# Kernel tuning notes

Measured on AMD Instinct MI355X. Metric: run time of the kernel, lower is better.

## Reference

```python
import jax, jax.numpy as jnp
import numpy as np

# Geometry (LLaMA-7B-like attention)
B, H, S, D = 1, 32, 2048, 128
NUM_ELEM = B * H * S * D
NUM_OUTLIERS = NUM_ELEM // 256   # outlier_ratio = 1/256 -> 32768 outliers
SINK_LENGTH = 4                  # first 4 tokens of V kept in full precision
QMAX = 7.0                       # symmetric int4: values in [-8, 7]
EPS = 1e-6


def setup_inputs() -> dict:
    key = jax.random.key(0)
    kq, kk, kv = jax.random.split(key, 3)
    q = jax.random.normal(kq, (B, H, S, D), dtype=jnp.float32)
    k = jax.random.normal(kk, (B, H, S, D), dtype=jnp.float32)
    v = jax.random.normal(kv, (B, H, S, D), dtype=jnp.float32)
    return {"q": q, "k": k, "v": v}


def _isolate(x):
    """Split x into dense (outliers zeroed) + sparse (top-|x| values, flat indices)."""
    flat = x.reshape(-1)
    _, idx = jax.lax.top_k(jnp.abs(flat), NUM_OUTLIERS)
    sp_val = flat[idx]
    dense = flat.at[idx].set(0.0).reshape(x.shape)
    return dense, sp_val, idx


def _sink_flat_indices():
    # flat indices of v[:, :, :SINK_LENGTH, :] in row-major [B,H,S,D] layout
    b = jnp.arange(B)[:, None, None, None]
    h = jnp.arange(H)[None, :, None, None]
    s = jnp.arange(SINK_LENGTH)[None, None, :, None]
    d = jnp.arange(D)[None, None, None, :]
    return (((b * H + h) * S + s) * D + d).reshape(-1)


def _quant_dequant(x, scale):
    # symmetric round-to-nearest int4 quantize, then dequantize
    q = jnp.clip(jnp.round(x / scale), -8.0, QMAX)
    return q * scale


def reference(q, k, v):
    # 1) Outlier isolation (K along tokens, V along channels; both flattened scatter)
    k_dense, k_sp_val, k_sp_idx = _isolate(k)
    v_dense, v_sp_val, v_sp_idx = _isolate(v)

    # 2) Sink-token isolation for V (chunk_idx == 0 path): zero sinks in dense,
    #    append their fp values/indices to the sparse set
    sink_idx = _sink_flat_indices()
    v_flat = v.reshape(-1)
    sink_values = v_flat[sink_idx]
    v_dense = v_dense.reshape(-1).at[sink_idx].set(0.0).reshape(v.shape)
    v_sp_val = jnp.concatenate([v_sp_val, sink_values])
    v_sp_idx = jnp.concatenate([v_sp_idx, sink_idx])

    # 3) Per-(head, channel) scale stats (EMA init == first-chunk max |.|)
    k_scale = jnp.maximum(jnp.max(jnp.abs(k_dense), axis=(0, 2), keepdims=True), EPS) / QMAX
    v_scale = jnp.maximum(jnp.max(jnp.abs(v_dense), axis=(0, 2), keepdims=True), EPS) / QMAX

    # 4) Quantize dense part, then reconstruct cache entries: dequant + sparse restore
    k_rec = _quant_dequant(k_dense, k_scale)
    v_rec = _quant_dequant(v_dense, v_scale)
    k_rec = k_rec.reshape(-1).at[k_sp_idx].set(k_sp_val).reshape(k.shape)
    v_rec = v_rec.reshape(-1).at[v_sp_idx].set(v_sp_val).reshape(v.shape)

    # 5) Causal attention over reconstructed KV cache
    scale = 1.0 / np.sqrt(D).astype(np.float32)
    scores = jnp.einsum('bhqd,bhkd->bhqk', q, k_rec) * scale
    causal = jnp.tril(jnp.ones((S, S), dtype=bool))
    scores = jnp.where(causal[None, None], scores, jnp.finfo(scores.dtype).min)
    attn = jax.nn.softmax(scores, axis=-1)
    out = jnp.einsum('bhqk,bhkd->bhqd', attn, v_rec)
    return out
```

## Files before the change

kernel.cpp:

```cpp
#include <hip/hip_runtime.h>

typedef unsigned short u16;
typedef unsigned int u32;
typedef unsigned long long u64;
typedef __attribute__((ext_vector_type(8))) short short8;
typedef __attribute__((ext_vector_type(4))) float f32x4;

#define N_ELEM 8388608
#define NH 32
#define SEQ 2048
#define HD 128
#define KTOP 32768u
#define CAND_CAP 8192u

__device__ __forceinline__ u16 f2bf(float f) {
  union { float f; u32 u; } v; v.f = f;
  u32 r = v.u + 0x7fffu + ((v.u >> 16) & 1u);
  return (u16)(r >> 16);
}

__device__ __forceinline__ float dqf(float x, u32 t, u64 Kr, u32 idx, bool sink, float scale) {
  union { float f; u32 u; } w; w.f = x;
  const u32 ab = w.u & 0x7fffffffu;
  const u32 bin = ab >> 16;
  const bool keep = sink || (bin > t) ||
                    (bin == t && ((((u64)ab) << 32) | (u32)(~idx)) >= Kr);
  if (keep) return x;
  float q = rintf(x / scale);
  q = fminf(fmaxf(q, -8.0f), 7.0f);
  return q * scale;
}

template<int CTRL>
__device__ __forceinline__ float dppmov(float x) {
  union { float f; int i; } a, b;
  a.f = x;
  b.i = __builtin_amdgcn_mov_dpp(a.i, CTRL, 0xF, 0xF, true);
  return b.f;
}
__device__ __forceinline__ float rowmax16(float x) {
  x = fmaxf(x, dppmov<0xB1>(x));
  x = fmaxf(x, dppmov<0x4E>(x));
  x = fmaxf(x, dppmov<0x141>(x));
  x = fmaxf(x, dppmov<0x140>(x));
  return x;
}
__device__ __forceinline__ float rowsum16(float x) {
  x += dppmov<0xB1>(x);
  x += dppmov<0x4E>(x);
  x += dppmov<0x141>(x);
  x += dppmov<0x140>(x);
  return x;
}

__global__ __launch_bounds__(256) void hist_kernel(const float* __restrict__ k,
                                                   const float* __restrict__ v,
                                                   u32* __restrict__ histK,
                                                   u32* __restrict__ histV) {
  __shared__ u32 sh[16384];
  const int tensor = blockIdx.x >> 7;
  const int bid = blockIdx.x & 127;
  const float* src = tensor ? v : k;
  u32* gh = tensor ? histV : histK;
  for (int i = threadIdx.x; i < 16384; i += 256) sh[i] = 0;
  __syncthreads();
  const int per = N_ELEM / 128;
  const int base = bid * per;
  for (int i = threadIdx.x; i < per / 4; i += 256) {
    f32x4 x = *(const f32x4*)(src + base + i * 4);
#pragma unroll
    for (int j = 0; j < 4; ++j) {
      union { float f; u32 u; } w; w.f = x[j];
      u32 b = (w.u & 0x7fffffffu) >> 16;
      atomicAdd(&sh[b >> 1], 1u << ((b & 1u) * 16));
    }
  }
  __syncthreads();
  for (int i = threadIdx.x; i < 16384; i += 256) {
    u32 w = sh[i];
    u32 lo = w & 0xffffu, hi = w >> 16;
    if (lo) atomicAdd(&gh[2 * i], lo);
    if (hi) atomicAdd(&gh[2 * i + 1], hi);
  }
}

__global__ __launch_bounds__(256) void thresh_kernel(const u32* __restrict__ histK,
                                                     const u32* __restrict__ histV,
                                                     u32* __restrict__ ctrl) {
  const u32* hist = blockIdx.x ? histV : histK;
  u32* c = ctrl + blockIdx.x * 8;
  __shared__ u32 part[256];
  __shared__ u32 bins[128];
  __shared__ u32 sh_chunk, sh_cum;
  u32 s = 0;
  for (int i = 0; i < 128; ++i) s += hist[threadIdx.x * 128 + i];
  part[threadIdx.x] = s;
  __syncthreads();
  if (threadIdx.x == 0) {
    u32 cum = 0;
    int chunk = 255;
    while (chunk > 0 && cum + part[chunk] < KTOP) { cum += part[chunk]; --chunk; }
    sh_chunk = (u32)chunk; sh_cum = cum;
  }
  __syncthreads();
  const u32 chunk = sh_chunk;
  if (threadIdx.x < 128) bins[threadIdx.x] = hist[chunk * 128 + threadIdx.x];
  __syncthreads();
  if (threadIdx.x == 0) {
    u32 cum = sh_cum;
    int b = 127;
    while (b > 0 && cum + bins[b] < KTOP) { cum += bins[b]; --b; }
    c[0] = chunk * 128 + (u32)b;
    c[1] = KTOP - cum;
  }
}

__global__ __launch_bounds__(256) void candmax_kernel(const float* __restrict__ k,
                                                      const float* __restrict__ v,
                                                      u32* __restrict__ ctrl,
                                                      u32* __restrict__ caK, u32* __restrict__ ciK,
                                                      u32* __restrict__ caV, u32* __restrict__ ciV,
                                                      u32* __restrict__ kmax,
                                                      u32* __restrict__ vmax) {
  __shared__ u32 colmax[128];
  const int tensor = blockIdx.y;
  const float* src = tensor ? v : k;
  u32* ca = tensor ? caV : caK;
  u32* ci = tensor ? ciV : ciK;
  u32* cnt = &ctrl[tensor * 8 + 4];
  u32* mbuf = tensor ? vmax : kmax;
  const u32 t = ctrl[tensor * 8 + 0];
  const int h = blockIdx.x >> 3;
  const int q8 = blockIdx.x & 7;
  const int tid = threadIdx.x;
  if (tid < 128) colmax[tid] = 0;
  __syncthreads();
  const int c0 = 4 * (tid & 31);
  u32 mx[4] = {0, 0, 0, 0};
  for (int p = 0; p < 32; ++p) {
    const int s = q8 * 256 + p * 8 + (tid >> 5);
    const u32 idx = ((u32)(h * SEQ + s) << 7) + (u32)c0;
    f32x4 x = *(const f32x4*)(src + idx);
    const bool skipmax = (tensor == 1 && s < 4);
#pragma unroll
    for (int j = 0; j < 4; ++j) {
      union { float f; u32 u; } w; w.f = x[j];
      const u32 ab = w.u & 0x7fffffffu;
      const u32 bin = ab >> 16;
      if (bin == t) {
        u32 slot = atomicAdd(cnt, 1u);
        if (slot < CAND_CAP) { ca[slot] = ab; ci[slot] = idx + j; }
      }
      if (bin < t && !skipmax && ab > mx[j]) mx[j] = ab;
    }
  }
#pragma unroll
  for (int j = 0; j < 4; ++j) atomicMax(&colmax[c0 + j], mx[j]);
  __syncthreads();
  if (tid < 128) atomicMax(&mbuf[h * HD + tid], colmax[tid]);
}

__global__ __launch_bounds__(256) void ksel_kernel(u32* __restrict__ ctrl,
                                                   const u32* __restrict__ caK, const u32* __restrict__ ciK,
                                                   const u32* __restrict__ caV, const u32* __restrict__ ciV) {
  __shared__ u64 keys[CAND_CAP];
  const int tensor = blockIdx.y;
  u32* c = ctrl + tensor * 8;
  const u32 r = c[1];
  u32 T = c[4];
  if (T > CAND_CAP) T = CAND_CAP;
  const u32* ca = tensor ? caV : caK;
  const u32* ci = tensor ? ciV : ciK;
  for (u32 j = threadIdx.x; j < T; j += 256)
    keys[j] = (((u64)ca[j]) << 32) | (u32)(~ci[j]);
  __syncthreads();
  for (u32 i = blockIdx.x * 256 + threadIdx.x; i < T; i += 32 * 256) {
    const u64 ki = keys[i];
    u32 cnt = 0;
    for (u32 j = 0; j < T; ++j) cnt += (keys[j] > ki) ? 1u : 0u;
    if (cnt == r - 1) { c[2] = (u32)(ki >> 32); c[3] = (u32)ki; }
  }
}

__global__ __launch_bounds__(256) void maxfix_scale_kernel(const u32* __restrict__ ctrl,
                                                           const u32* __restrict__ caK, const u32* __restrict__ ciK,
                                                           const u32* __restrict__ caV, const u32* __restrict__ ciV,
                                                           u32* __restrict__ kmax, u32* __restrict__ vmax,
                                                           float* __restrict__ kscale, float* __restrict__ vscale) {
  const int tensor = blockIdx.x;
  const u32* c = ctrl + tensor * 8;
  const u64 Kr = (((u64)c[2]) << 32) | c[3];
  u32 T = c[4];
  if (T > CAND_CAP) T = CAND_CAP;
  const u32* ca = tensor ? caV : caK;
  const u32* ci = tensor ? ciV : ciK;
  u32* mbuf = tensor ? vmax : kmax;
  for (u32 i = threadIdx.x; i < T; i += 256) {
    const u32 ab = ca[i], idx = ci[i];
    const u64 key = (((u64)ab) << 32) | (u32)(~idx);
    if (key >= Kr) continue;
    if (tensor == 1 && ((idx >> 7) & 2047) < 4) continue;
    atomicMax(&mbuf[(idx >> 18) * HD + (idx & 127)], ab);
  }
  __syncthreads();
  float* sbuf = tensor ? vscale : kscale;
  for (int i = threadIdx.x; i < NH * HD; i += 256) {
    union { u32 u; float f; } a; a.u = mbuf[i];
    sbuf[i] = fmaxf(a.f, 1e-6f) / 7.0f;
  }
}

__global__ __launch_bounds__(256) void recon_k_kernel(const float* __restrict__ K,
                                                      const u32* __restrict__ ctrl,
                                                      const float* __restrict__ kscale,
                                                      u16* __restrict__ krec) {
  const u32 t = ctrl[0];
  const u64 Kr = (((u64)ctrl[2]) << 32) | ctrl[3];
  const int stride = gridDim.x * 256;
  for (int i = blockIdx.x * 256 + threadIdx.x; i < N_ELEM / 4; i += stride) {
    const u32 e = (u32)i * 4;
    const u32 d0 = e & 127, h = e >> 18;
    f32x4 x = *(const f32x4*)(K + e);
    f32x4 sc = *(const f32x4*)(kscale + h * HD + d0);
    u16 y[4];
#pragma unroll
    for (int j = 0; j < 4; ++j) y[j] = f2bf(dqf(x[j], t, Kr, e + j, false, sc[j]));
    *(u32*)(krec + e) = ((u32)y[0]) | (((u32)y[1]) << 16);
    *(u32*)(krec + e + 2) = ((u32)y[2]) | (((u32)y[3]) << 16);
  }
}

__global__ __launch_bounds__(256) void recon_vt_kernel(const float* __restrict__ V,
                                                       const u32* __restrict__ ctrl,
                                                       const float* __restrict__ vscale,
                                                       u16* __restrict__ vrecT) {
  __shared__ u32 ld[64][65];
  const u32 t = ctrl[8];
  const u64 Kr = (((u64)ctrl[10]) << 32) | ctrl[11];
  const int h = blockIdx.x, sb = blockIdx.y;
  const int tid = threadIdx.x;
  const int d0 = 4 * (tid & 31);
  f32x4 sc = *(const f32x4*)(vscale + h * HD + d0);
#pragma unroll
  for (int p = 0; p < 8; ++p) {
    const int sl = p * 8 + (tid >> 5);
    const int tok = sb * 64 + sl;
    const bool sink = tok < 4;
    const u32 idx = ((u32)(h * SEQ + tok) << 7) + (u32)d0;
    f32x4 x = *(const f32x4*)(V + idx);
    u16 y[4];
#pragma unroll
    for (int j = 0; j < 4; ++j) y[j] = f2bf(dqf(x[j], t, Kr, idx + j, sink, sc[j]));
    ld[(d0 >> 1)][sl] = ((u32)y[0]) | (((u32)y[1]) << 16);
    ld[(d0 >> 1) + 1][sl] = ((u32)y[2]) | (((u32)y[3]) << 16);
  }
  __syncthreads();
  const int d = tid >> 1, so = (tid & 1) * 32, e = d & 1;
  u16* outp = vrecT + (size_t)(h * 32 + sb) * 8192 + d * 64 + so;
#pragma unroll
  for (int i = 0; i < 4; ++i) {
    short8 y;
#pragma unroll
    for (int m = 0; m < 8; ++m) {
      const u32 w2 = ld[d >> 1][so + i * 8 + m];
      y[m] = (short)(u16)(w2 >> (16 * e));
    }
    *(short8*)(outp + i * 8) = y;
  }
}

__global__ __launch_bounds__(256, 2) void flash_pre(const float* __restrict__ Q,
                                                    const u16* __restrict__ krec,
                                                    const u16* __restrict__ vrecT,
                                                    float* __restrict__ Out) {
  __shared__ u16 ks[64][136];
  __shared__ u16 vt[128][72];
  __shared__ u16 pl[4][16][72];

  const int blk = blockIdx.x;
  const int h = blk >> 4;
  const int pa = blk & 15;
  const int RA = pa << 6;
  const int RB = (31 - pa) << 6;
  const int tid = threadIdx.x;
  const int w = tid >> 6, lane = tid & 63;
  const int l16 = lane & 15, quad = lane >> 4;
  const float SC = 0.12751743f;
  const float NEG = -30000.0f;

  short8 qf[2][4];
#pragma unroll
  for (int m = 0; m < 2; ++m) {
    const int R = m ? RB : RA;
    const float* qp = Q + ((size_t)(h * SEQ + R + w * 16 + l16)) * HD + quad * 8;
#pragma unroll
    for (int c = 0; c < 4; ++c) {
      f32x4 a = *(const f32x4*)(qp + c * 32);
      f32x4 b = *(const f32x4*)(qp + c * 32 + 4);
#pragma unroll
      for (int j = 0; j < 4; ++j) {
        qf[m][c][j] = (short)f2bf(a[j]);
        qf[m][c][4 + j] = (short)f2bf(b[j]);
      }
    }
  }

  f32x4 o[2][8];
  float mrow[2][4], lrow[2][4];
#pragma unroll
  for (int m = 0; m < 2; ++m) {
#pragma unroll
    for (int i = 0; i < 8; ++i) o[m][i] = (f32x4){0.f, 0.f, 0.f, 0.f};
#pragma unroll
    for (int r = 0; r < 4; ++r) { mrow[m][r] = NEG; lrow[m][r] = 0.f; }
  }

  const int krow = tid >> 2, kqo = (tid & 3) * 32;
  const int vd = tid >> 1, vso = (tid & 1) * 32;
  const u16* kbase = krec + ((size_t)h * SEQ + krow) * HD + kqo;
  const u16* vbase = vrecT + (size_t)h * 32 * 8192 + vd * 64 + vso;
  short8 kr[4], vr[4];
#pragma unroll
  for (int i = 0; i < 4; ++i) kr[i] = *(const short8*)(kbase + i * 8);
#pragma unroll
  for (int i = 0; i < 4; ++i) vr[i] = *(const short8*)(vbase + i * 8);

  const int ktiles = (RB >> 6) + 1;
  for (int kt = 0; kt < ktiles; ++kt) {
    const int kb = kt << 6;
    __syncthreads();
#pragma unroll
    for (int i = 0; i < 4; ++i) *(short8*)(&ks[krow][kqo + i * 8]) = kr[i];
#pragma unroll
    for (int i = 0; i < 4; ++i) *(short8*)(&vt[vd][vso + i * 8]) = vr[i];
    __syncthreads();
    if (kt + 1 < ktiles) {
      const u16* kp = kbase + (size_t)(kt + 1) * 64 * HD;
      const u16* vp = vbase + (size_t)(kt + 1) * 8192;
#pragma unroll
      for (int i = 0; i < 4; ++i) kr[i] = *(const short8*)(kp + i * 8);
#pragma unroll
      for (int i = 0; i < 4; ++i) vr[i] = *(const short8*)(vp + i * 8);
    }
#pragma unroll
    for (int m = 0; m < 2; ++m) {
      const int R = m ? RB : RA;
      if (kb > R) continue;
      f32x4 sa[4];
#pragma unroll
      for (int ni = 0; ni < 4; ++ni) {
        f32x4 acc = (f32x4){0.f, 0.f, 0.f, 0.f};
#pragma unroll
        for (int c = 0; c < 4; ++c) {
          short8 kf = *(const short8*)(&ks[ni * 16 + l16][c * 32 + quad * 8]);
          acc = __builtin_amdgcn_mfma_f32_16x16x32_bf16(qf[m][c], kf, acc, 0, 0, 0);
        }
        sa[ni] = acc;
      }
      const bool diag = (kb == R);
#pragma unroll
      for (int ni = 0; ni < 4; ++ni)
#pragma unroll
        for (int r = 0; r < 4; ++r) {
          float sv = sa[ni][r] * SC;
          if (diag && (ni * 16 + l16) > (w * 16 + quad * 4 + r)) sv = NEG;
          sa[ni][r] = sv;
        }
      float alpha[4];
#pragma unroll
      for (int r = 0; r < 4; ++r) {
        float mx = fmaxf(fmaxf(sa[0][r], sa[1][r]), fmaxf(sa[2][r], sa[3][r]));
        mx = rowmax16(mx);
        const float mn = fmaxf(mrow[m][r], mx);
        alpha[r] = exp2f(mrow[m][r] - mn);
        mrow[m][r] = mn;
        float sum = 0.f;
#pragma unroll
        for (int ni = 0; ni < 4; ++ni) {
          const float p = exp2f(sa[ni][r] - mn);
          sa[ni][r] = p;
          sum += p;
        }
        sum = rowsum16(sum);
        lrow[m][r] = lrow[m][r] * alpha[r] + sum;
      }
#pragma unroll
      for (int ni = 0; ni < 4; ++ni)
#pragma unroll
        for (int r = 0; r < 4; ++r)
          pl[w][quad * 4 + r][ni * 16 + l16] = f2bf(sa[ni][r]);
#pragma unroll
      for (int i = 0; i < 8; ++i)
#pragma unroll
        for (int r = 0; r < 4; ++r) o[m][i][r] *= alpha[r];
#pragma unroll
      for (int kc = 0; kc < 2; ++kc) {
        short8 af = *(const short8*)(&pl[w][l16][kc * 32 + quad * 8]);
#pragma unroll
        for (int ds = 0; ds < 8; ++ds) {
          short8 vf = *(const short8*)(&vt[ds * 16 + l16][kc * 32 + quad * 8]);
          o[m][ds] = __builtin_amdgcn_mfma_f32_16x16x32_bf16(af, vf, o[m][ds], 0, 0, 0);
        }
      }
    }
  }
#pragma unroll
  for (int m = 0; m < 2; ++m) {
    const int R = m ? RB : RA;
#pragma unroll
    for (int r = 0; r < 4; ++r) {
      const float inv = 1.0f / lrow[m][r];
      const int qr = R + w * 16 + quad * 4 + r;
      float* op = Out + ((size_t)(h * SEQ + qr)) * HD + l16;
#pragma unroll
      for (int ds = 0; ds < 8; ++ds) op[ds * 16] = o[m][ds][r] * inv;
    }
  }
}

__global__ __launch_bounds__(256, 2) void flash_fb(const float* __restrict__ Q,
                                                   const float* __restrict__ K,
                                                   const float* __restrict__ V,
                                                   const u32* __restrict__ ctrl,
                                                   const float* __restrict__ kscale,
                                                   const float* __restrict__ vscale,
                                                   float* __restrict__ Out) {
  __shared__ u16 ks[64][136];
  __shared__ u16 vt[128][72];
  __shared__ u16 pl[4][16][72];
  const int blk = blockIdx.x;
  const int h = blk >> 5;
  const int qt = 31 - (blk & 31);
  const int qb = qt << 6;
  const int tid = threadIdx.x;
  const int w = tid >> 6, lane = tid & 63;
  const int l16 = lane & 15, quad = lane >> 4;
  const float SM_SCALE = 0.08838834764831843f;
  const float NEG = -30000.0f;
  const u32 tK = ctrl[0];
  const u64 KrK = (((u64)ctrl[2]) << 32) | ctrl[3];
  const u32 tV = ctrl[8];
  const u64 KrV = (((u64)ctrl[10]) << 32) | ctrl[11];
  const int cch = (tid & 15) * 8;
  float ksc[8], vsc[8];
#pragma unroll
  for (int j = 0; j < 8; ++j) {
    ksc[j] = kscale[h * HD + cch + j];
    vsc[j] = vscale[h * HD + cch + j];
  }
  short8 qf[4];
  {
    const float* qp = Q + ((size_t)(h * SEQ + qb + w * 16 + l16)) * HD + quad * 8;
#pragma unroll
    for (int c = 0; c < 4; ++c) {
      f32x4 a = *(const f32x4*)(qp + c * 32);
      f32x4 b = *(const f32x4*)(qp + c * 32 + 4);
#pragma unroll
      for (int j = 0; j < 4; ++j) {
        qf[c][j] = (short)f2bf(a[j]);
        qf[c][4 + j] = (short)f2bf(b[j]);
      }
    }
  }
  f32x4 o[8];
#pragma unroll
  for (int i = 0; i < 8; ++i) o[i] = (f32x4){0.f, 0.f, 0.f, 0.f};
  float mrow[4], lrow[4];
#pragma unroll
  for (int r = 0; r < 4; ++r) { mrow[r] = NEG; lrow[r] = 0.f; }
  const int ktiles = qt + 1;
  for (int kt = 0; kt < ktiles; ++kt) {
    const int kb = kt << 6;
    __syncthreads();
    {
      const int r0 = tid >> 4;
      const float* kp = K + (size_t)(h * SEQ + kb) * HD;
#pragma unroll
      for (int i = 0; i < 4; ++i) {
        const int row = r0 + i * 16;
        f32x4 x0 = *(const f32x4*)(kp + (size_t)row * HD + cch);
        f32x4 x1 = *(const f32x4*)(kp + (size_t)row * HD + cch + 4);
        const u32 bidx = ((u32)(h * SEQ + kb + row) << 7) + (u32)cch;
        short8 yv;
#pragma unroll
        for (int j = 0; j < 4; ++j) {
          yv[j]     = (short)f2bf(dqf(x0[j], tK, KrK, bidx + j,     false, ksc[j]));
          yv[4 + j] = (short)f2bf(dqf(x1[j], tK, KrK, bidx + 4 + j, false, ksc[4 + j]));
        }
        *(short8*)(&ks[row][cch]) = yv;
      }
    }
    {
      const float* vp = V + (size_t)(h * SEQ + kb) * HD;
#pragma unroll
      for (int i = 0; i < 4; ++i) {
        const int tchunk = tid + i * 256;
        const int s = tchunk >> 4;
        const int tok = kb + s;
        const bool sink = tok < 4;
        f32x4 x0 = *(const f32x4*)(vp + (size_t)s * HD + cch);
        f32x4 x1 = *(const f32x4*)(vp + (size_t)s * HD + cch + 4);
        const u32 bidx = ((u32)(h * SEQ + tok) << 7) + (u32)cch;
#pragma unroll
        for (int j = 0; j < 4; ++j) {
          vt[cch + j][s]     = f2bf(dqf(x0[j], tV, KrV, bidx + j,     sink, vsc[j]));
          vt[cch + 4 + j][s] = f2bf(dqf(x1[j], tV, KrV, bidx + 4 + j, sink, vsc[4 + j]));
        }
      }
    }
    __syncthreads();
    f32x4 sa[4];
#pragma unroll
    for (int ni = 0; ni < 4; ++ni) {
      f32x4 acc = (f32x4){0.f, 0.f, 0.f, 0.f};
#pragma unroll
      for (int c = 0; c < 4; ++c) {
        short8 kf = *(const short8*)(&ks[ni * 16 + l16][c * 32 + quad * 8]);
        acc = __builtin_amdgcn_mfma_f32_16x16x32_bf16(qf[c], kf, acc, 0, 0, 0);
      }
      sa[ni] = acc;
    }
    const bool diag = (kb == qb);
#pragma unroll
    for (int ni = 0; ni < 4; ++ni)
#pragma unroll
      for (int r = 0; r < 4; ++r) {
        float sv = sa[ni][r] * SM_SCALE;
        if (diag) {
          const int qr = w * 16 + quad * 4 + r;
          const int kc = ni * 16 + l16;
          if (kc > qr) sv = NEG;
        }
        sa[ni][r] = sv;
      }
    float alpha[4];
#pragma unroll
    for (int r = 0; r < 4; ++r) {
      float mx = fmaxf(fmaxf(sa[0][r], sa[1][r]), fmaxf(sa[2][r], sa[3][r]));
      mx = fmaxf(mx, __shfl_xor(mx, 1));
      mx = fmaxf(mx, __shfl_xor(mx, 2));
      mx = fmaxf(mx, __shfl_xor(mx, 4));
      mx = fmaxf(mx, __shfl_xor(mx, 8));
      const float mn = fmaxf(mrow[r], mx);
      alpha[r] = __expf(mrow[r] - mn);
      mrow[r] = mn;
      float sum = 0.f;
#pragma unroll
      for (int ni = 0; ni < 4; ++ni) {
        const float p = __expf(sa[ni][r] - mn);
        sa[ni][r] = p;
        sum += p;
      }
      sum += __shfl_xor(sum, 1);
      sum += __shfl_xor(sum, 2);
      sum += __shfl_xor(sum, 4);
      sum += __shfl_xor(sum, 8);
      lrow[r] = lrow[r] * alpha[r] + sum;
    }
#pragma unroll
    for (int ni = 0; ni < 4; ++ni)
#pragma unroll
      for (int r = 0; r < 4; ++r)
        pl[w][quad * 4 + r][ni * 16 + l16] = f2bf(sa[ni][r]);
    __syncthreads();
#pragma unroll
    for (int i = 0; i < 8; ++i)
#pragma unroll
      for (int r = 0; r < 4; ++r) o[i][r] *= alpha[r];
#pragma unroll
    for (int kc = 0; kc < 2; ++kc) {
      short8 af = *(const short8*)(&pl[w][l16][kc * 32 + quad * 8]);
#pragma unroll
      for (int ds = 0; ds < 8; ++ds) {
        short8 vf = *(const short8*)(&vt[ds * 16 + l16][kc * 32 + quad * 8]);
        o[ds] = __builtin_amdgcn_mfma_f32_16x16x32_bf16(af, vf, o[ds], 0, 0, 0);
      }
    }
  }
#pragma unroll
  for (int r = 0; r < 4; ++r) {
    const float inv = 1.0f / lrow[r];
    const int qr = qb + w * 16 + quad * 4 + r;
    float* op = Out + ((size_t)(h * SEQ + qr)) * HD + l16;
#pragma unroll
    for (int ds = 0; ds < 8; ++ds) op[ds * 16] = o[ds][r] * inv;
  }
}

extern "C" void kernel_launch(void* const* d_in, const int* in_sizes, int n_in,
                              void* d_out, int out_size, void* d_ws, size_t ws_size,
                              hipStream_t stream) {
  const float* q = (const float*)d_in[0];
  const float* k = (const float*)d_in[1];
  const float* v = (const float*)d_in[2];
  float* out = (float*)d_out;
  char* ws = (char*)d_ws;

  u32* ctrl    = (u32*)ws;
  u32* histK   = (u32*)(ws + 256);
  u32* histV   = (u32*)(ws + 256 + 131072);
  u32* kmax    = (u32*)(ws + 262400);
  u32* vmax    = (u32*)(ws + 278784);
  const size_t ZERO_BYTES = 295168;
  float* kscale = (float*)(ws + 295168);
  float* vscale = (float*)(ws + 311552);
  u32* caK = (u32*)(ws + 327936);
  u32* ciK = caK + CAND_CAP;
  u32* caV = ciK + CAND_CAP;
  u32* ciV = caV + CAND_CAP;
  u16* krec  = (u16*)(ws + 458752);
  u16* vrecT = (u16*)(ws + 458752 + 16777216);
  const size_t NEED = 458752 + 2ull * 16777216;

  hipMemsetAsync(ws, 0, ZERO_BYTES, stream);
  hist_kernel<<<256, 256, 0, stream>>>(k, v, histK, histV);
  thresh_kernel<<<2, 256, 0, stream>>>(histK, histV, ctrl);
  candmax_kernel<<<dim3(256, 2), 256, 0, stream>>>(k, v, ctrl, caK, ciK, caV, ciV, kmax, vmax);
  ksel_kernel<<<dim3(32, 2), 256, 0, stream>>>(ctrl, caK, ciK, caV, ciV);
  maxfix_scale_kernel<<<2, 256, 0, stream>>>(ctrl, caK, ciK, caV, ciV, kmax, vmax, kscale, vscale);
  if (ws_size >= NEED) {
    recon_k_kernel<<<2048, 256, 0, stream>>>(k, ctrl, kscale, krec);
    recon_vt_kernel<<<dim3(32, 32), 256, 0, stream>>>(v, ctrl, vscale, vrecT);
    flash_pre<<<512, 256, 0, stream>>>(q, krec, vrecT, out);
  } else {
    flash_fb<<<32 * 32, 256, 0, stream>>>(q, k, v, ctrl, kscale, vscale, out);
  }
}
```

Before: 362.3 us.

## Compute transposed S tile so P stays in registers, dropping the LDS round-trip

Flash_pre now computes S^T with K as the A operand, so each lane owns one query row. Row max and sum need only two cross-lane shuffles, and P is packed to bf16 with v_cvt_pk_bf16_f32 and fed straight into the PV MFMA, removing the pl shared-memory staging. K rows are permuted when written to LDS so the register layout of P lines up with the V operand. The two query tiles are interleaved to raise MFMA ILP, and alpha and l are redistributed with ds_bpermute, at the cost of more register pressure and a subtle layout permutation that must stay correct.

```diff
diff --git a/kernel.cpp b/kernel.cpp
--- a/kernel.cpp
+++ b/kernel.cpp
@@ -31,26 +31,17 @@
   return q * scale;
 }
 
-template<int CTRL>
-__device__ __forceinline__ float dppmov(float x) {
+__device__ __forceinline__ u32 cvtpk_bf16(float lo, float hi) {
+  u32 r;
+  asm("v_cvt_pk_bf16_f32 %0, %1, %2" : "=v"(r) : "v"(lo), "v"(hi));
+  return r;
+}
+
+__device__ __forceinline__ float bperm_f(int ibyte, float x) {
   union { float f; int i; } a, b;
   a.f = x;
-  b.i = __builtin_amdgcn_mov_dpp(a.i, CTRL, 0xF, 0xF, true);
+  b.i = __builtin_amdgcn_ds_bpermute(ibyte, a.i);
   return b.f;
-}
-__device__ __forceinline__ float rowmax16(float x) {
-  x = fmaxf(x, dppmov<0xB1>(x));
-  x = fmaxf(x, dppmov<0x4E>(x));
-  x = fmaxf(x, dppmov<0x141>(x));
-  x = fmaxf(x, dppmov<0x140>(x));
-  return x;
-}
-__device__ __forceinline__ float rowsum16(float x) {
-  x += dppmov<0xB1>(x);
-  x += dppmov<0x4E>(x);
-  x += dppmov<0x141>(x);
-  x += dppmov<0x140>(x);
-  return x;
 }
 
 __global__ __launch_bounds__(256) void hist_kernel(const float* __restrict__ k,
@@ -269,13 +260,58 @@
   }
 }
 
+#define SC_QK 0.12751743f
+#define NEGS -30000.0f
+
+__device__ __forceinline__ void softmax_pack(f32x4 s[4], float& mrow, float& lrow,
+                                             u32 pk[8], f32x4& av, bool diag,
+                                             int qrow16, int quad, const int* idxR) {
+#pragma unroll
+  for (int ni = 0; ni < 4; ++ni)
+#pragma unroll
+    for (int r = 0; r < 4; ++r) {
+      float sv = s[ni][r] * SC_QK;
+      const int tokl = ((ni >> 1) << 5) | (quad << 3) | ((ni & 1) << 2) | r;
+      if (diag && tokl > qrow16) sv = NEGS;
+      s[ni][r] = sv;
+    }
+  float m01 = fmaxf(fmaxf(fmaxf(s[0][0], s[0][1]), fmaxf(s[0][2], s[0][3])),
+                    fmaxf(fmaxf(s[1][0], s[1][1]), fmaxf(s[1][2], s[1][3])));
+  float m23 = fmaxf(fmaxf(fmaxf(s[2][0], s[2][1]), fmaxf(s[2][2], s[2][3])),
+                    fmaxf(fmaxf(s[3][0], s[3][1]), fmaxf(s[3][2], s[3][3])));
+  float mx = fmaxf(m01, m23);
+  mx = fmaxf(mx, __shfl_xor(mx, 16));
+  mx = fmaxf(mx, __shfl_xor(mx, 32));
+  const float mn = fmaxf(mrow, mx);
+  const float al = exp2f(mrow - mn);
+  mrow = mn;
+  float sum = 0.f;
+#pragma unroll
+  for (int ni = 0; ni < 4; ++ni)
+#pragma unroll
+    for (int r = 0; r < 4; ++r) {
+      const float p = exp2f(s[ni][r] - mn);
+      s[ni][r] = p;
+      sum += p;
+    }
+  sum += __shfl_xor(sum, 16);
+  sum += __shfl_xor(sum, 32);
+  lrow = lrow * al + sum;
+#pragma unroll
+  for (int ni = 0; ni < 4; ++ni) {
+    pk[ni * 2] = cvtpk_bf16(s[ni][0], s[ni][1]);
+    pk[ni * 2 + 1] = cvtpk_bf16(s[ni][2], s[ni][3]);
+  }
+#pragma unroll
+  for (int r = 0; r < 4; ++r) av[r] = bperm_f(idxR[r], al);
+}
+
 __global__ __launch_bounds__(256, 2) void flash_pre(const float* __restrict__ Q,
                                                     const u16* __restrict__ krec,
                                                     const u16* __restrict__ vrecT,
                                                     float* __restrict__ Out) {
   __shared__ u16 ks[64][136];
   __shared__ u16 vt[128][72];
-  __shared__ u16 pl[4][16][72];
 
   const int blk = blockIdx.x;
   const int h = blk >> 4;
@@ -285,8 +321,11 @@
   const int tid = threadIdx.x;
   const int w = tid >> 6, lane = tid & 63;
   const int l16 = lane & 15, quad = lane >> 4;
-  const float SC = 0.12751743f;
-  const float NEG = -30000.0f;
+  const int qrow16 = w * 16 + l16;
+
+  int idxR[4];
+#pragma unroll
+  for (int r = 0; r < 4; ++r) idxR[r] = ((lane & 48) | (quad * 4 + r)) << 2;
 
   short8 qf[2][4];
 #pragma unroll
@@ -297,25 +336,27 @@
     for (int c = 0; c < 4; ++c) {
       f32x4 a = *(const f32x4*)(qp + c * 32);
       f32x4 b = *(const f32x4*)(qp + c * 32 + 4);
-#pragma unroll
-      for (int j = 0; j < 4; ++j) {
-        qf[m][c][j] = (short)f2bf(a[j]);
-        qf[m][c][4 + j] = (short)f2bf(b[j]);
-      }
+      union { u32 u[4]; short8 v; } t;
+      t.u[0] = cvtpk_bf16(a[0], a[1]);
+      t.u[1] = cvtpk_bf16(a[2], a[3]);
+      t.u[2] = cvtpk_bf16(b[0], b[1]);
+      t.u[3] = cvtpk_bf16(b[2], b[3]);
+      qf[m][c] = t.v;
     }
   }
 
   f32x4 o[2][8];
-  float mrow[2][4], lrow[2][4];
+  float mrow[2], lrow[2];
 #pragma unroll
   for (int m = 0; m < 2; ++m) {
 #pragma unroll
     for (int i = 0; i < 8; ++i) o[m][i] = (f32x4){0.f, 0.f, 0.f, 0.f};
-#pragma unroll
-    for (int r = 0; r < 4; ++r) { mrow[m][r] = NEG; lrow[m][r] = 0.f; }
+    mrow[m] = NEGS; lrow[m] = 0.f;
   }
 
   const int krow = tid >> 2, kqo = (tid & 3) * 32;
+  const int krp = (krow & 35) | (((krow >> 2) & 1) << 4) |
+                  (((krow >> 4) & 1) << 3) | (((krow >> 3) & 1) << 2);
   const int vd = tid >> 1, vso = (tid & 1) * 32;
   const u16* kbase = krec + ((size_t)h * SEQ + krow) * HD + kqo;
   const u16* vbase = vrecT + (size_t)h * 32 * 8192 + vd * 64 + vso;
@@ -330,7 +371,7 @@
     const int kb = kt << 6;
     __syncthreads();
 #pragma unroll
-    for (int i = 0; i < 4; ++i) *(short8*)(&ks[krow][kqo + i * 8]) = kr[i];
+    for (int i = 0; i < 4; ++i) *(short8*)(&ks[krp][kqo + i * 8]) = kr[i];
 #pragma unroll
     for (int i = 0; i < 4; ++i) *(short8*)(&vt[vd][vso + i * 8]) = vr[i];
     __syncthreads();
@@ -342,78 +383,89 @@
 #pragma unroll
       for (int i = 0; i < 4; ++i) vr[i] = *(const short8*)(vp + i * 8);
     }
-#pragma unroll
-    for (int m = 0; m < 2; ++m) {
-      const int R = m ? RB : RA;
-      if (kb > R) continue;
-      f32x4 sa[4];
+    const bool actA = (kb <= RA);
+
+    f32x4 s0[4], s1[4];
+    if (actA) {
 #pragma unroll
       for (int ni = 0; ni < 4; ++ni) {
-        f32x4 acc = (f32x4){0.f, 0.f, 0.f, 0.f};
+        f32x4 a0 = (f32x4){0.f, 0.f, 0.f, 0.f};
+        f32x4 a1 = (f32x4){0.f, 0.f, 0.f, 0.f};
 #pragma unroll
         for (int c = 0; c < 4; ++c) {
           short8 kf = *(const short8*)(&ks[ni * 16 + l16][c * 32 + quad * 8]);
-          acc = __builtin_amdgcn_mfma_f32_16x16x32_bf16(qf[m][c], kf, acc, 0, 0, 0);
+          a0 = __builtin_amdgcn_mfma_f32_16x16x32_bf16(kf, qf[0][c], a0, 0, 0, 0);
+          a1 = __builtin_amdgcn_mfma_f32_16x16x32_bf16(kf, qf[1][c], a1, 0, 0, 0);
         }
-        sa[ni] = acc;
-      }
-      const bool diag = (kb == R);
-#pragma unroll
-      for (int ni = 0; ni < 4; ++ni)
-#pragma unroll
-        for (int r = 0; r < 4; ++r) {
-          float sv = sa[ni][r] * SC;
-          if (diag && (ni * 16 + l16) > (w * 16 + quad * 4 + r)) sv = NEG;
-          sa[ni][r] = sv;
+        s0[ni] = a0; s1[ni] = a1;
+      }
+    } else {
+#pragma unroll
+      for (int ni = 0; ni < 4; ++ni) {
+        f32x4 a1 = (f32x4){0.f, 0.f, 0.f, 0.f};
+#pragma unroll
+        for (int c = 0; c < 4; ++c) {
+          short8 kf = *(const short8*)(&ks[ni * 16 + l16][c * 32 + quad * 8]);
+          a1 = __builtin_amdgcn_mfma_f32_16x16x32_bf16(kf, qf[1][c], a1, 0, 0, 0);
         }
-      float alpha[4];
-#pragma unroll
-      for (int r = 0; r < 4; ++r) {
-        float mx = fmaxf(fmaxf(sa[0][r], sa[1][r]), fmaxf(sa[2][r], sa[3][r]));
-        mx = rowmax16(mx);
-        const float mn = fmaxf(mrow[m][r], mx);
-        alpha[r] = exp2f(mrow[m][r] - mn);
-        mrow[m][r] = mn;
-        float sum = 0.f;
-#pragma unroll
-        for (int ni = 0; ni < 4; ++ni) {
-          const float p = exp2f(sa[ni][r] - mn);
-          sa[ni][r] = p;
-          sum += p;
-        }
-        sum = rowsum16(sum);
-        lrow[m][r] = lrow[m][r] * alpha[r] + sum;
-      }
-#pragma unroll
-      for (int ni = 0; ni < 4; ++ni)
-#pragma unroll
-        for (int r = 0; r < 4; ++r)
-          pl[w][quad * 4 + r][ni * 16 + l16] = f2bf(sa[ni][r]);
-#pragma unroll
-      for (int i = 0; i < 8; ++i)
-#pragma unroll
-        for (int r = 0; r < 4; ++r) o[m][i][r] *= alpha[r];
+        s1[ni] = a1;
+      }
+    }
+
+    u32 pk0[8], pk1[8];
+    f32x4 av0, av1;
+    if (actA) softmax_pack(s0, mrow[0], lrow[0], pk0, av0, kb == RA, qrow16, quad, idxR);
+    softmax_pack(s1, mrow[1], lrow[1], pk1, av1, kb == RB, qrow16, quad, idxR);
+
+    if (actA) {
+#pragma unroll
+      for (int i = 0; i < 8; ++i) o[0][i] *= av0;
+    }
+#pragma unroll
+    for (int i = 0; i < 8; ++i) o[1][i] *= av1;
+
+    if (actA) {
 #pragma unroll
       for (int kc = 0; kc < 2; ++kc) {
-        short8 af = *(const short8*)(&pl[w][l16][kc * 32 + quad * 8]);
+        union { u32 u[4]; short8 v; } a0u, a1u;
+#pragma unroll
+        for (int t = 0; t < 4; ++t) { a0u.u[t] = pk0[kc * 4 + t]; a1u.u[t] = pk1[kc * 4 + t]; }
+        const short8 af0 = a0u.v, af1 = a1u.v;
 #pragma unroll
         for (int ds = 0; ds < 8; ++ds) {
           short8 vf = *(const short8*)(&vt[ds * 16 + l16][kc * 32 + quad * 8]);
-          o[m][ds] = __builtin_amdgcn_mfma_f32_16x16x32_bf16(af, vf, o[m][ds], 0, 0, 0);
+          o[0][ds] = __builtin_amdgcn_mfma_f32_16x16x32_bf16(af0, vf, o[0][ds], 0, 0, 0);
+          o[1][ds] = __builtin_amdgcn_mfma_f32_16x16x32_bf16(af1, vf, o[1][ds], 0, 0, 0);
         }
       }
-    }
-  }
+    } else {
+#pragma unroll
+      for (int kc = 0; kc < 2; ++kc) {
+        union { u32 u[4]; short8 v; } a1u;
+#pragma unroll
+        for (int t = 0; t < 4; ++t) a1u.u[t] = pk1[kc * 4 + t];
+        const short8 af1 = a1u.v;
+#pragma unroll
+        for (int ds = 0; ds < 8; ++ds) {
+          short8 vf = *(const short8*)(&vt[ds * 16 + l16][kc * 32 + quad * 8]);
+          o[1][ds] = __builtin_amdgcn_mfma_f32_16x16x32_bf16(af1, vf, o[1][ds], 0, 0, 0);
+        }
+      }
+    }
+  }
+
 #pragma unroll
   for (int m = 0; m < 2; ++m) {
     const int R = m ? RB : RA;
+    float linv[4];
+#pragma unroll
+    for (int r = 0; r < 4; ++r) linv[r] = 1.0f / bperm_f(idxR[r], lrow[m]);
 #pragma unroll
     for (int r = 0; r < 4; ++r) {
-      const float inv = 1.0f / lrow[m][r];
       const int qr = R + w * 16 + quad * 4 + r;
       float* op = Out + ((size_t)(h * SEQ + qr)) * HD + l16;
 #pragma unroll
-      for (int ds = 0; ds < 8; ++ds) op[ds * 16] = o[m][ds][r] * inv;
+      for (int ds = 0; ds < 8; ++ds) op[ds * 16] = o[m][ds][r] * linv[r];
     }
   }
 }
```

Measured after the change: 365.1 us. No clear change (+0.8%).
